# Performance work log

Measured on AMD Instinct MI355X. Metric: run time of the kernel, lower is better.

The kernel has to match this reference:

```python
import jax, jax.numpy as jnp
import numpy as np

N = 32       # number of variables (per-var LSTMs)
L = 128      # window length
D = 128      # hidden dim
HEADS = 8
TAU_MAX = 5
ALPHA = 0.7  # attn_decay_alpha
B = 128      # number of time-ordered windows


def setup_inputs() -> dict:
    key = jax.random.key(0)
    ks = jax.random.split(key, 20)
    s = 0.1
    f = lambda k, shape: (jax.random.normal(k, shape, jnp.float32) * s)
    return {
        "X": jax.random.normal(ks[0], (B, L, N), jnp.float32),
        # per-variable encoder LSTM (input size 1): W_ih (N,4D), W_hh (N,4D,D), combined-style biases kept separate
        "enc_Wih": f(ks[1], (N, 4 * D)),
        "enc_Whh": f(ks[2], (N, 4 * D, D)),
        "enc_b": f(ks[3], (N, 4 * D)),            # b_ih + b_hh merged (mathematically identical)
        "pool_w": f(ks[4], (N, D)),
        "pool_b": f(ks[5], (N,)),
        # shared MultiheadAttention params (torch layout: in_proj (3D,D))
        "in_proj_w": f(ks[6], (3 * D, D)),
        "in_proj_b": f(ks[7], (3 * D,)),
        "out_proj_w": f(ks[8], (D, D)),
        "out_proj_b": f(ks[9], (D,)),
        # per-variable decoder: init_h/init_c Linear(d,d), LSTM(1,d) (input is all-zeros so W_ih drops out), out Linear(d,1)
        "dec_initH_w": f(ks[10], (N, D, D)),
        "dec_initH_b": f(ks[11], (N, D)),
        "dec_initC_w": f(ks[12], (N, D, D)),
        "dec_initC_b": f(ks[13], (N, D)),
        "dec_Whh": f(ks[14], (N, 4 * D, D)),
        "dec_bih": f(ks[15], (N, 4 * D)),
        "dec_bhh": f(ks[16], (N, 4 * D)),
        "dec_out_w": f(ks[17], (N, D)),
        "dec_out_b": f(ks[18], (N,)),
    }


def _lstm_cell(gates, c):
    # torch gate order: i, f, g, o
    i, fg, g, o = jnp.split(gates, 4, axis=-1)
    i = jax.nn.sigmoid(i); fg = jax.nn.sigmoid(fg)
    g = jnp.tanh(g); o = jax.nn.sigmoid(o)
    c = fg * c + i * g
    h = o * jnp.tanh(c)
    return h, c


def _encode(X, Wih, Whh, b, pool_w, pool_b):
    # X: (B,L,N); encoder consumes first L-1 steps of each variable, batched over all N vars
    x = jnp.transpose(X[:, :-1, :], (1, 2, 0))  # (T, N, B)
    Bn = X.shape[0]
    h0 = jnp.zeros((N, Bn, D), X.dtype)

    def step(carry, x_t):  # x_t: (N,B)
        h, c = carry
        gates = (x_t[..., None] * Wih[:, None, :]
                 + jnp.einsum('nbd,ngd->nbg', h, Whh)
                 + b[:, None, :])
        h, c = _lstm_cell(gates, c)
        return (h, c), h

    _, H = jax.lax.scan(step, (h0, h0), x)  # H: (T,N,B,D)
    # TemporalAttnPool: softmax over time of a linear score, weighted sum
    scores = jnp.einsum('tnbd,nd->tnb', H, pool_w) + pool_b[None, :, None]
    a = jax.nn.softmax(scores, axis=0)
    C = jnp.einsum('tnb,tnbd->bnd', a, H)  # (B,N,D)
    return C


def _mha(Q, KV, in_w, in_b, out_w, out_b):
    dh = D // HEADS
    q = Q @ in_w[:D].T + in_b[:D]
    k = KV @ in_w[D:2 * D].T + in_b[D:2 * D]
    v = KV @ in_w[2 * D:].T + in_b[2 * D:]
    sp = lambda x: x.reshape(x.shape[0], x.shape[1], HEADS, dh)
    q, k, v = sp(q), sp(k), sp(v)
    scores = jnp.einsum('bqhd,bkhd->bhqk', q, k) / float(np.sqrt(dh))
    attn = jax.nn.softmax(scores, axis=-1)
    o = jnp.einsum('bhqk,bkhd->bqhd', attn, v).reshape(Q.shape)
    return o @ out_w.T + out_b


def _cross_attend(C, in_w, in_b, out_w, out_b):
    Bn = C.shape[0]
    tmax = min(TAU_MAX, Bn - 1)
    if tmax <= 0:
        return C
    out_sum = jnp.zeros_like(C)
    w_sum = jnp.zeros((Bn, 1, 1), C.dtype)
    for tau in range(1, tmax + 1):  # small fixed loop over lags
        o = _mha(C[tau:], C[:-tau], in_w, in_b, out_w, out_b)
        w = float(np.exp(-ALPHA * (tau - 1)))  # attn_agg == 'decay'
        out_sum = out_sum.at[tau:].add(o * w)
        w_sum = w_sum.at[tau:].add(w)
    out = out_sum / jnp.clip(w_sum, 1e-8)
    return C + out  # residual=True


def _decode(C_star, iHw, iHb, iCw, iCb, Whh, bih, bhh, ow, ob):
    # h0/c0 from tanh(Linear(c_star)); LSTM input is all-zeros so input term reduces to b_ih
    h0 = jnp.tanh(jnp.einsum('bnd,ned->nbe', C_star, iHw) + iHb[:, None, :])
    c0 = jnp.tanh(jnp.einsum('bnd,ned->nbe', C_star, iCw) + iCb[:, None, :])
    b = (bih + bhh)[:, None, :]  # (N,1,4D)

    def step(carry, _):
        h, c = carry
        gates = jnp.einsum('nbd,ngd->nbg', h, Whh) + b
        h, c = _lstm_cell(gates, c)
        o = jnp.einsum('nbd,nd->nb', h, ow) + ob[:, None]
        return (h, c), o

    _, O = jax.lax.scan(step, (h0, c0), None, length=L)  # (L,N,B)
    recon = jnp.transpose(O[:L - 1], (2, 0, 1))  # (B,L-1,N)
    pred = O[L - 1].T                            # (B,N)
    return recon, pred


def reference(X, enc_Wih, enc_Whh, enc_b, pool_w, pool_b,
              in_proj_w, in_proj_b, out_proj_w, out_proj_b,
              dec_initH_w, dec_initH_b, dec_initC_w, dec_initC_b,
              dec_Whh, dec_bih, dec_bhh, dec_out_w, dec_out_b):
    C = _encode(X, enc_Wih, enc_Whh, enc_b, pool_w, pool_b)
    C_star = _cross_attend(C, in_proj_w, in_proj_b, out_proj_w, out_proj_b)
    recon, pred = _decode(C_star, dec_initH_w, dec_initH_b, dec_initC_w, dec_initC_b,
                          dec_Whh, dec_bih, dec_bhh, dec_out_w, dec_out_b)
    return recon, pred, C_star
```

## Files before the change

### kernel.cpp

```cpp
#include <hip/hip_runtime.h>
#include <hip/hip_bf16.h>

typedef unsigned short ushort_t;
typedef unsigned int uint_t;

#define DD   128
#define G4   512
#define BT   16
#define NB   128
#define NV   32

#define OFF_WIH   0
#define OFF_EB    16384
#define OFF_PW    32768
#define OFF_PB    36864
#define OFF_INW   37120
#define OFF_INB   86272
#define OFF_OUTW  86784
#define OFF_OUTB  103168
#define OFF_IHB   103424
#define OFF_ICB   107520
#define OFF_DBIH  111616
#define OFF_DBHH  128000
#define OFF_DOW   144384
#define OFF_DOB   148480
#define P_TOTAL   148736
#define OFF_FLAGS (OFF_PB + 32)

typedef __attribute__((ext_vector_type(8))) short bf16x8;
typedef __attribute__((ext_vector_type(4))) float f32x4;

__device__ __forceinline__ float bf2f(ushort_t u) {
    union { uint_t i; float f; } x; x.i = ((uint_t)u) << 16; return x.f;
}
__device__ __forceinline__ ushort_t f2bf(float f) {
    __hip_bfloat16 h = __float2bfloat16(f);
    return *(ushort_t*)&h;
}
__device__ __forceinline__ float f2u_f(float f) { return f; }
__device__ __forceinline__ uint_t f2u(float f) {
    union { float f; uint_t i; } x; x.f = f; return x.i;
}
__device__ __forceinline__ float u2f(uint_t u) {
    union { uint_t i; float f; } x; x.i = u; return x.f;
}
__device__ __forceinline__ float exp2_f(float x) {
    float r; asm("v_exp_f32 %0, %1" : "=v"(r) : "v"(x)); return r;
}
__device__ __forceinline__ float sigmoid_f(float x) {
    return __builtin_amdgcn_rcpf(1.f + exp2_f(x * -1.442695041f));
}
__device__ __forceinline__ float tanh_f(float x) {
    return 1.f - 2.f * __builtin_amdgcn_rcpf(exp2_f(x * 2.885390082f) + 1.f);
}
__device__ __forceinline__ uint_t cvt_pk_bf16(float a, float b) {
    uint_t r; asm("v_cvt_pk_bf16_f32 %0, %1, %2" : "=v"(r) : "v"(a), "v"(b)); return r;
}
__device__ __forceinline__ bf16x8 pack8(f32x4 a, f32x4 b) {
    union { uint_t u[4]; bf16x8 v; } x;
    x.u[0] = cvt_pk_bf16(a.x, a.y); x.u[1] = cvt_pk_bf16(a.z, a.w);
    x.u[2] = cvt_pk_bf16(b.x, b.y); x.u[3] = cvt_pk_bf16(b.z, b.w);
    return x.v;
}
__device__ __forceinline__ float swz_bcast_l15(float v) {
    return u2f((uint_t)__builtin_amdgcn_ds_swizzle((int)f2u(v), 0x000F));
}
__device__ __forceinline__ void store_out(void* out, long idx, float v, int bf) {
    if (bf) ((ushort_t*)out)[idx] = f2bf(v);
    else    ((float*)out)[idx]    = v;
}
#define LBAR() do { asm volatile("s_waitcnt lgkmcnt(0)" ::: "memory"); \
                    __builtin_amdgcn_s_barrier(); } while (0)

__device__ __forceinline__ int wave_probe(const void* p, int elems) {
    int cap = elems < 2048 ? elems : 2048;
    int lane = threadIdx.x & 63;
    const ushort_t* u = (const ushort_t*)p;
    int cnt = 0, tot = 0;
    for (int j = lane; j < cap; j += 64) {
        ushort_t x = u[j];
        float af = fabsf(bf2f(x));
        tot++;
        if (x == 0 || (af > 1e-7f && af < 100.f)) cnt++;
    }
    #pragma unroll
    for (int off = 32; off >= 1; off >>= 1) {
        cnt += __shfl_xor(cnt, off);
        tot += __shfl_xor(tot, off);
    }
    return (cnt * 10 >= tot * 9) ? 1 : 0;
}

struct Ptr19 { const void* p[19]; };

__global__ __launch_bounds__(256) void prep_kernel(Ptr19 a, float* __restrict__ P,
                                                   float* __restrict__ Xc) {
    __shared__ float tile[32][65];
    if (blockIdx.x < 581) {
        int base = blockIdx.x * 256;
        int src, o0, size;
        if      (base < OFF_EB)   { src = 1;  o0 = base - OFF_WIH;  size = 16384; }
        else if (base < OFF_PW)   { src = 3;  o0 = base - OFF_EB;   size = 16384; }
        else if (base < OFF_PB)   { src = 4;  o0 = base - OFF_PW;   size = 4096;  }
        else if (base < OFF_INW)  { src = 5;  o0 = base - OFF_PB;   size = 32;    }
        else if (base < OFF_INB)  { src = 6;  o0 = base - OFF_INW;  size = 49152; }
        else if (base < OFF_OUTW) { src = 7;  o0 = base - OFF_INB;  size = 384;   }
        else if (base < OFF_OUTB) { src = 8;  o0 = base - OFF_OUTW; size = 16384; }
        else if (base < OFF_IHB)  { src = 9;  o0 = base - OFF_OUTB; size = 128;   }
        else if (base < OFF_ICB)  { src = 11; o0 = base - OFF_IHB;  size = 4096;  }
        else if (base < OFF_DBIH) { src = 13; o0 = base - OFF_ICB;  size = 4096;  }
        else if (base < OFF_DBHH) { src = 15; o0 = base - OFF_DBIH; size = 16384; }
        else if (base < OFF_DOW)  { src = 16; o0 = base - OFF_DBHH; size = 16384; }
        else if (base < OFF_DOB)  { src = 17; o0 = base - OFF_DOW;  size = 4096;  }
        else                      { src = 18; o0 = base - OFF_DOB;  size = 32;    }
        int bf = wave_probe(a.p[src], size);
        int off = o0 + (int)threadIdx.x;
        if (off < size)
            P[base + threadIdx.x] = bf ? bf2f(((const ushort_t*)a.p[src])[off])
                                       : ((const float*)a.p[src])[off];
    } else if (blockIdx.x < 837) {
        int bf = wave_probe(a.p[0], 2048);
        int idx2 = blockIdx.x - 581;
        int bt = (idx2 & 3) * 32, tn0 = (idx2 >> 2) * 64;
        const void* src = a.p[0];
        int tx = threadIdx.x & 63, ty = threadIdx.x >> 6;
        #pragma unroll
        for (int k = 0; k < 8; k++) {
            int row = ty * 8 + k;
            int idx = (bt + row) * 4096 + tn0 + tx;
            tile[row][tx] = bf ? bf2f(((const ushort_t*)src)[idx]) : ((const float*)src)[idx];
        }
        __syncthreads();
        int bx = threadIdx.x & 31, tyy = threadIdx.x >> 5;
        #pragma unroll
        for (int k = 0; k < 8; k++) {
            int tn = tn0 + tyy * 8 + k;
            int t = tn >> 5, nn = tn & 31;
            Xc[t * 4096 + nn * 128 + bt + bx] = tile[bx][tyy * 8 + k];
        }
    } else {
        int which = blockIdx.x - 837;
        int src = (which == 0) ? 0 : (which == 1) ? 2 : (which == 2) ? 10
                : (which == 3) ? 12 : 14;
        int flag = wave_probe(a.p[src], 2048);
        if (threadIdx.x == 0) P[OFF_FLAGS + which] = (float)flag;
    }
}

__global__ __launch_bounds__(512, 2) void enc_kernel(
    const float* __restrict__ Xc, const void* __restrict__ Wraw,
    const float* __restrict__ P, float* __restrict__ Cout)
{
    const int n = blockIdx.y, b0 = blockIdx.x * BT;
    const int tid = threadIdx.x;
    const int w = tid >> 6, lane = tid & 63;
    const int l15 = lane & 15, quad = lane >> 4;
    const int wbf = P[OFF_FLAGS + 1] > 0.5f;
    const int bown = b0 + l15;

    __shared__ alignas(16) ushort_t hS[2][16 * 136];
    for (int i = tid; i < 16 * 136; i += 512) hS[0][i] = 0;

    bf16x8 afrag[4][4];
    #pragma unroll
    for (int typ = 0; typ < 4; typ++) {
        const int g = typ * 128 + 16 * w + l15;
        #pragma unroll
        for (int kc = 0; kc < 4; kc++) {
            const int base = (n * G4 + g) * DD + 32 * kc + 8 * quad;
            if (wbf) {
                afrag[typ][kc] = *(const bf16x8*)((const ushort_t*)Wraw + base);
            } else {
                const float* fp = (const float*)Wraw + base;
                afrag[typ][kc] = pack8(*(const f32x4*)fp, *(const f32x4*)(fp + 4));
            }
        }
    }

    bf16x8 pfrag[4];
    #pragma unroll
    for (int kc = 0; kc < 4; kc++) {
        bf16x8 tmp;
        #pragma unroll
        for (int j = 0; j < 8; j++)
            tmp[j] = (l15 == 0 || l15 == 8)
                   ? (short)f2bf(P[OFF_PW + n * DD + 32 * kc + 8 * quad + j]) : (short)0;
        pfrag[kc] = tmp;
    }

    f32x4 bias4[4], wih4[4];
    #pragma unroll
    for (int typ = 0; typ < 4; typ++) {
        int base = n * G4 + typ * 128 + 16 * w + 4 * quad;
        bias4[typ] = *(const f32x4*)&P[OFF_EB + base];
        wih4[typ]  = *(const f32x4*)&P[OFF_WIH + base];
    }
    const float pb_r = P[OFF_PB + n];
    const f32x4 pb4 = {pb_r, pb_r, pb_r, pb_r};

    float cst[4] = {0.f, 0.f, 0.f, 0.f};
    f32x4 hprev = {0.f, 0.f, 0.f, 0.f};
    f32x4 Cacc  = {0.f, 0.f, 0.f, 0.f};
    float lR = 0.f;

    const float* xnext = Xc + n * 128 + bown;
    float xq = *xnext;
    xnext += 4096;

#define ENC_STEP(T, RB)                                                              \
    do {                                                                             \
        LBAR();                                                                      \
        bf16x8 bh[4];                                                                \
        _Pragma("unroll")                                                            \
        for (int kc = 0; kc < 4; kc++)                                               \
            bh[kc] = *(const bf16x8*)&hS[RB][l15 * 136 + 32 * kc + 8 * quad];        \
        f32x4 xv = {xq, xq, xq, xq};                                                 \
        f32x4 acc[4];                                                                \
        _Pragma("unroll")                                                            \
        for (int typ = 0; typ < 4; typ++)                                            \
            acc[typ] = __builtin_amdgcn_mfma_f32_16x16x32_bf16(                      \
                afrag[typ][0], bh[0], bias4[typ] + xv * wih4[typ], 0, 0, 0);         \
        f32x4 accP = __builtin_amdgcn_mfma_f32_16x16x32_bf16(pfrag[0], bh[0], pb4, 0, 0, 0); \
        xq = *xnext; xnext += 4096;    \
        _Pragma("unroll")                                                            \
        for (int kc = 1; kc < 4; kc++) {                                             \
            accP = __builtin_amdgcn_mfma_f32_16x16x32_bf16(pfrag[kc], bh[kc], accP, 0, 0, 0); \
            _Pragma("unroll")                                                        \
            for (int typ = 0; typ < 4; typ++)                                        \
                acc[typ] = __builtin_amdgcn_mfma_f32_16x16x32_bf16(afrag[typ][kc], bh[kc], acc[typ], 0, 0, 0); \
        }                                                                            \
        if ((T) > 0) {                                                               \
            float e = __expf(swz_bcast_l15(accP[0]));                                \
            lR += e;                                                                 \
            f32x4 ev = {e, e, e, e};                                                 \
            Cacc += ev * hprev;                                                      \
        }                                                                            \
        float hh[4];                                                                 \
        _Pragma("unroll")                                                            \
        for (int r = 0; r < 4; r++) {                                                \
            float ii = sigmoid_f(acc[0][r]);                                         \
            float ff = sigmoid_f(acc[1][r]);                                         \
            float g2 = tanh_f(acc[2][r]);                                            \
            float oo = sigmoid_f(acc[3][r]);                                         \
            float cc = ff * cst[r] + ii * g2;                                        \
            cst[r] = cc;                                                             \
            hh[r] = oo * tanh_f(cc);                                                 \
        }                                                                            \
        hprev.x = hh[0]; hprev.y = hh[1]; hprev.z = hh[2]; hprev.w = hh[3];          \
        uint2 hw;                                                                    \
        hw.x = cvt_pk_bf16(hh[0], hh[1]);                                            \
        hw.y = cvt_pk_bf16(hh[2], hh[3]);                                            \
        *(uint2*)&hS[(RB) ^ 1][l15 * 136 + 16 * w + 4 * quad] = hw;                  \
    } while (0)

    for (int tp = 0; tp < 63; tp++) {
        ENC_STEP(2 * tp, 0);
        ENC_STEP(2 * tp + 1, 1);
    }
    ENC_STEP(126, 0);
#undef ENC_STEP

    LBAR();
    {
        f32x4 accP = __builtin_amdgcn_mfma_f32_16x16x32_bf16(
            pfrag[0], *(const bf16x8*)&hS[1][l15 * 136 + 8 * quad], pb4, 0, 0, 0);
        #pragma unroll
        for (int kc = 1; kc < 4; kc++) {
            bf16x8 bh = *(const bf16x8*)&hS[1][l15 * 136 + 32 * kc + 8 * quad];
            accP = __builtin_amdgcn_mfma_f32_16x16x32_bf16(pfrag[kc], bh, accP, 0, 0, 0);
        }
        float e = __expf(swz_bcast_l15(accP[0]));
        lR += e;
        f32x4 ev = {e, e, e, e};
        Cacc += ev * hprev;
    }
    float inv = 1.f / lR;
    f32x4 iv = {inv, inv, inv, inv};
    f32x4 cv = Cacc * iv;
    *(f32x4*)&Cout[bown * (NV * DD) + n * DD + 16 * w + 4 * quad] = cv;
}

__global__ __launch_bounds__(256) void qkv_kernel(
    const float* __restrict__ C, const float* __restrict__ P,
    float* __restrict__ q, float* __restrict__ k, float* __restrict__ v)
{
    int b = blockIdx.x, p = blockIdx.y, tid = threadIdx.x;
    int j = tid & 127, half = tid >> 7;
    __shared__ float Cb[NV * DD];
    for (int i = tid; i < NV * DD; i += 256) Cb[i] = C[b * (NV * DD) + i];
    __syncthreads();

    const float* wrow = P + OFF_INW + (p * DD + j) * DD;
    float bias = P[OFF_INB + p * DD + j];
    float acc[16];
    #pragma unroll
    for (int nn = 0; nn < 16; nn++) acc[nn] = bias;

    for (int dc = 0; dc < DD; dc += 8) {
        float4 w0 = *(const float4*)&wrow[dc];
        float4 w1 = *(const float4*)&wrow[dc + 4];
        #pragma unroll
        for (int nn = 0; nn < 16; nn++) {
            const float* cb = &Cb[(half * 16 + nn) * DD + dc];
            float4 c0 = *(float4*)&cb[0];
            float4 c1 = *(float4*)&cb[4];
            acc[nn] += c0.x * w0.x + c0.y * w0.y + c0.z * w0.z + c0.w * w0.w
                     + c1.x * w1.x + c1.y * w1.y + c1.z * w1.z + c1.w * w1.w;
        }
    }
    float* dst = (p == 0) ? q : (p == 1) ? k : v;
    for (int nn = 0; nn < 16; nn++)
        dst[b * (NV * DD) + (half * 16 + nn) * DD + j] = acc[nn];
}

__global__ __launch_bounds__(128) void attn_kernel(
    const float* __restrict__ q, const float* __restrict__ k, const float* __restrict__ v,
    const float* __restrict__ C, const float* __restrict__ P,
    float* __restrict__ Cstar, void* __restrict__ dout)
{
    int b = blockIdx.x, half = blockIdx.y, tid = threadIdx.x;
    int obf = P[OFF_FLAGS + 0] > 0.5f;
    int n0 = half * 16;
    __shared__ float Qs[16 * DD], Ks[NV * DD], Vs[NV * DD];
    float* Os = Ks;
    for (int i = tid; i < 16 * DD; i += 128) Qs[i] = q[b * (NV * DD) + n0 * DD + i];
    __syncthreads();

    int hh = tid >> 4, qi = tid & 15;
    float qreg[16];
    #pragma unroll
    for (int u = 0; u < 4; u++) {
        float4 t4 = *(float4*)&Qs[qi * DD + hh * 16 + 4 * u];
        qreg[4*u] = t4.x; qreg[4*u+1] = t4.y; qreg[4*u+2] = t4.z; qreg[4*u+3] = t4.w;
    }

    float Oacc[16];
    #pragma unroll
    for (int u = 0; u < 16; u++) Oacc[u] = 0.f;
    float wsum = 0.f;
    int tmax = (b < 5) ? b : 5;

    for (int tau = 1; tau <= tmax; tau++) {
        __syncthreads();
        for (int i = tid; i < NV * DD; i += 128) {
            Ks[i] = k[(b - tau) * (NV * DD) + i];
            Vs[i] = v[(b - tau) * (NV * DD) + i];
        }
        __syncthreads();

        float s[NV];
        #pragma unroll
        for (int kk = 0; kk < NV; kk++) {
            float a = 0.f;
            #pragma unroll
            for (int u = 0; u < 4; u++) {
                float4 kv = *(float4*)&Ks[kk * DD + hh * 16 + 4 * u];
                a += qreg[4*u] * kv.x + qreg[4*u+1] * kv.y
                   + qreg[4*u+2] * kv.z + qreg[4*u+3] * kv.w;
            }
            s[kk] = a * 0.25f;
        }
        float mm = s[0];
        #pragma unroll
        for (int kk = 1; kk < NV; kk++) mm = fmaxf(mm, s[kk]);
        float ssum = 0.f;
        #pragma unroll
        for (int kk = 0; kk < NV; kk++) { s[kk] = __expf(s[kk] - mm); ssum += s[kk]; }
        float wdk = __expf(-0.7f * (float)(tau - 1));
        wsum += wdk;
        float wr = wdk / ssum;
        #pragma unroll
        for (int u = 0; u < 4; u++) {
            float ax = 0.f, ay = 0.f, az = 0.f, aw = 0.f;
            #pragma unroll
            for (int kk = 0; kk < NV; kk++) {
                float4 vv = *(float4*)&Vs[kk * DD + hh * 16 + 4 * u];
                ax += s[kk] * vv.x; ay += s[kk] * vv.y;
                az += s[kk] * vv.z; aw += s[kk] * vv.w;
            }
            Oacc[4*u] += wr * ax; Oacc[4*u+1] += wr * ay;
            Oacc[4*u+2] += wr * az; Oacc[4*u+3] += wr * aw;
        }
    }

    __syncthreads();
    float winv = (b > 0) ? 1.f / wsum : 0.f;
    #pragma unroll
    for (int u = 0; u < 16; u++)
        Os[qi * DD + hh * 16 + u] = Oacc[u] * winv;
    __syncthreads();

    int j = tid;
    const float* wrow = P + OFF_OUTW + j * DD;
    float obias = P[OFF_OUTB + j];
    for (int nn = 0; nn < 16; nn++) {
        float a = (b > 0) ? obias : 0.f;
        for (int dc = 0; dc < DD; dc += 8) {
            float4 w0 = *(const float4*)&wrow[dc];
            float4 w1 = *(const float4*)&wrow[dc + 4];
            float4 o0 = *(float4*)&Os[nn * DD + dc];
            float4 o1 = *(float4*)&Os[nn * DD + dc + 4];
            a += o0.x*w0.x + o0.y*w0.y + o0.z*w0.z + o0.w*w0.w
               + o1.x*w1.x + o1.y*w1.y + o1.z*w1.z + o1.w*w1.w;
        }
        int nng = n0 + nn;
        float cs = C[b * (NV * DD) + nng * DD + j] + a;
        Cstar[b * (NV * DD) + nng * DD + j] = cs;
        store_out(dout, 524288 + b * (NV * DD) + nng * DD + j, cs, obf);
    }
}

__global__ __launch_bounds__(512, 2) void dec_kernel(
    const float* __restrict__ Cstar,
    const void* __restrict__ iHw, const void* __restrict__ iCw,
    const void* __restrict__ Wraw,
    const float* __restrict__ P, void* __restrict__ out)
{
    const int n = blockIdx.y, b0 = blockIdx.x * BT;
    const int tid = threadIdx.x;
    const int w = tid >> 6, lane = tid & 63;
    const int l15 = lane & 15, quad = lane >> 4;
    const int obf = P[OFF_FLAGS + 0] > 0.5f;
    const int hbf = P[OFF_FLAGS + 2] > 0.5f;
    const int cbf = P[OFF_FLAGS + 3] > 0.5f;
    const int wbf = P[OFF_FLAGS + 4] > 0.5f;
    const int bown = b0 + l15;

    __shared__ alignas(16) ushort_t hS[2][16 * 136];

    bf16x8 cstB[4];
    #pragma unroll
    for (int kc = 0; kc < 4; kc++) {
        const float* cp = &Cstar[bown * (NV * DD) + n * DD + 32 * kc + 8 * quad];
        cstB[kc] = pack8(*(const f32x4*)&cp[0], *(const f32x4*)&cp[4]);
    }
    float cst[4];
    {
        f32x4 hAcc = *(const f32x4*)&P[OFF_IHB + n * DD + 16 * w + 4 * quad];
        f32x4 cAcc = *(const f32x4*)&P[OFF_ICB + n * DD + 16 * w + 4 * quad];
        #pragma unroll
        for (int kc = 0; kc < 4; kc++) {
            const int base = (n * DD + 16 * w + l15) * DD + 32 * kc + 8 * quad;
            bf16x8 wA;
            if (hbf) wA = *(const bf16x8*)((const ushort_t*)iHw + base);
            else {
                const float* fp = (const float*)iHw + base;
                wA = pack8(*(const f32x4*)fp, *(const f32x4*)(fp + 4));
            }
            hAcc = __builtin_amdgcn_mfma_f32_16x16x32_bf16(wA, cstB[kc], hAcc, 0, 0, 0);
            if (cbf) wA = *(const bf16x8*)((const ushort_t*)iCw + base);
            else {
                const float* fp = (const float*)iCw + base;
                wA = pack8(*(const f32x4*)fp, *(const f32x4*)(fp + 4));
            }
            cAcc = __builtin_amdgcn_mfma_f32_16x16x32_bf16(wA, cstB[kc], cAcc, 0, 0, 0);
        }
        float h0 = tanh_f(hAcc[0]), h1 = tanh_f(hAcc[1]);
        float h2 = tanh_f(hAcc[2]), h3 = tanh_f(hAcc[3]);
        #pragma unroll
        for (int r = 0; r < 4; r++) cst[r] = tanh_f(cAcc[r]);
        uint2 hw;
        hw.x = cvt_pk_bf16(h0, h1);
        hw.y = cvt_pk_bf16(h2, h3);
        *(uint2*)&hS[0][l15 * 136 + 16 * w + 4 * quad] = hw;
    }

    bf16x8 afrag[4][4];
    #pragma unroll
    for (int typ = 0; typ < 4; typ++) {
        const int g = typ * 128 + 16 * w + l15;
        #pragma unroll
        for (int kc = 0; kc < 4; kc++) {
            const int base = (n * G4 + g) * DD + 32 * kc + 8 * quad;
            if (wbf) {
                afrag[typ][kc] = *(const bf16x8*)((const ushort_t*)Wraw + base);
            } else {
                const float* fp = (const float*)Wraw + base;
                afrag[typ][kc] = pack8(*(const f32x4*)fp, *(const f32x4*)(fp + 4));
            }
        }
    }

    bf16x8 pfrag[4];
    #pragma unroll
    for (int kc = 0; kc < 4; kc++) {
        bf16x8 tmp;
        #pragma unroll
        for (int j = 0; j < 8; j++)
            tmp[j] = (l15 == 0) ? (short)f2bf(P[OFF_DOW + n * DD + 32 * kc + 8 * quad + j]) : (short)0;
        pfrag[kc] = tmp;
    }

    f32x4 bias4[4];
    #pragma unroll
    for (int typ = 0; typ < 4; typ++) {
        int base = n * G4 + typ * 128 + 16 * w + 4 * quad;
        f32x4 b1 = *(const f32x4*)&P[OFF_DBIH + base];
        f32x4 b2 = *(const f32x4*)&P[OFF_DBHH + base];
        bias4[typ] = b1 + b2;
    }
    const float ob_r = P[OFF_DOB + n];
    const f32x4 ob4 = {ob_r, ob_r, ob_r, ob_r};

#define DEC_STEP(T, RB)                                                              \
    do {                                                                             \
        LBAR();                                                                      \
        bf16x8 bh[4];                                                                \
        _Pragma("unroll")                                                            \
        for (int kc = 0; kc < 4; kc++)                                               \
            bh[kc] = *(const bf16x8*)&hS[RB][l15 * 136 + 32 * kc + 8 * quad];        \
        f32x4 acc[4];                                                                \
        _Pragma("unroll")                                                            \
        for (int typ = 0; typ < 4; typ++)                                            \
            acc[typ] = __builtin_amdgcn_mfma_f32_16x16x32_bf16(afrag[typ][0], bh[0], bias4[typ], 0, 0, 0); \
        _Pragma("unroll")                                                            \
        for (int kc = 1; kc < 4; kc++)                                               \
            _Pragma("unroll")                                                        \
            for (int typ = 0; typ < 4; typ++)                                        \
                acc[typ] = __builtin_amdgcn_mfma_f32_16x16x32_bf16(afrag[typ][kc], bh[kc], acc[typ], 0, 0, 0); \
        if (w == ((T) & 7)) {    \
            f32x4 accP = __builtin_amdgcn_mfma_f32_16x16x32_bf16(pfrag[0], bh[0], ob4, 0, 0, 0); \
            _Pragma("unroll")                                                        \
            for (int kc = 1; kc < 4; kc++)                                           \
                accP = __builtin_amdgcn_mfma_f32_16x16x32_bf16(pfrag[kc], bh[kc], accP, 0, 0, 0); \
            if ((T) > 0 && quad == 0)                                                \
                store_out(out, (long)bown * 4064 + (long)((T) - 1) * NV + n, accP[0], obf); \
        }                                                                            \
        float hh[4];                                                                 \
        _Pragma("unroll")                                                            \
        for (int r = 0; r < 4; r++) {                                                \
            float ii = sigmoid_f(acc[0][r]);                                         \
            float ff = sigmoid_f(acc[1][r]);                                         \
            float g2 = tanh_f(acc[2][r]);                                            \
            float oo = sigmoid_f(acc[3][r]);                                         \
            float cc = ff * cst[r] + ii * g2;                                        \
            cst[r] = cc;                                                             \
            hh[r] = oo * tanh_f(cc);                                                 \
        }                                                                            \
        uint2 hw;                                                                    \
        hw.x = cvt_pk_bf16(hh[0], hh[1]);                                            \
        hw.y = cvt_pk_bf16(hh[2], hh[3]);                                            \
        *(uint2*)&hS[(RB) ^ 1][l15 * 136 + 16 * w + 4 * quad] = hw;                  \
    } while (0)

    for (int tp = 0; tp < 64; tp++) {
        DEC_STEP(2 * tp, 0);
        DEC_STEP(2 * tp + 1, 1);
    }
#undef DEC_STEP

    LBAR();
    if (w == 0) {
        f32x4 accP = __builtin_amdgcn_mfma_f32_16x16x32_bf16(
            pfrag[0], *(const bf16x8*)&hS[0][l15 * 136 + 8 * quad], ob4, 0, 0, 0);
        #pragma unroll
        for (int kc = 1; kc < 4; kc++) {
            bf16x8 bh = *(const bf16x8*)&hS[0][l15 * 136 + 32 * kc + 8 * quad];
            accP = __builtin_amdgcn_mfma_f32_16x16x32_bf16(pfrag[kc], bh, accP, 0, 0, 0);
        }
        if (quad == 0)
            store_out(out, 520192 + (long)bown * NV + n, accP[0], obf);
    }
}

extern "C" void kernel_launch(void* const* d_in, const int* in_sizes, int n_in,
                              void* d_out, int out_size, void* d_ws, size_t ws_size,
                              hipStream_t stream) {
    char* ws = (char*)d_ws;
    float*    P    = (float*)(ws + 0);
    float*    Xc   = (float*)(ws + (1u << 20));
    float*    C    = (float*)(ws + (3u << 20));
    float*    qb   = (float*)(ws + (5u << 20));
    float*    kb   = (float*)(ws + (7u << 20));
    float*    vb   = (float*)(ws + (9u << 20));
    float*    Cst  = (float*)(ws + (11u << 20));

    Ptr19 a;
    for (int i = 0; i < 19; i++) a.p[i] = d_in[i];

    prep_kernel<<<842, 256, 0, stream>>>(a, P, Xc);
    enc_kernel<<<dim3(8, 32), 512, 0, stream>>>(Xc, d_in[2], P, C);
    qkv_kernel<<<dim3(128, 3), 256, 0, stream>>>(C, P, qb, kb, vb);
    attn_kernel<<<dim3(128, 2), 128, 0, stream>>>(qb, kb, vb, C, P, Cst, d_out);
    dec_kernel<<<dim3(8, 32), 512, 0, stream>>>(Cst, d_in[10], d_in[12], d_in[14], P, d_out);
}
```

Before: 420.7 us.

## Compute pooling/output projections from fp32 hidden state via LDS atomics

Replaces the per-step MFMA-based pooling score (encoder) and output projection (decoder) with a per-lane fp32 dot product over each wave's own hidden slice, reduced by lane shuffles and LDS atomicAdd into a triple-buffered scratch row. The result is consumed one step later after the existing barrier. This removes the extra MFMA chain and the register fragments it needed from the serial recurrence. In exchange it adds shared-memory atomics and a rotating zero/accumulate/read buffer scheme. The projection now uses fp32 instead of bf16-rounded h, which changes rounding slightly.

Result: slower. 460.1 us (+9.4%).

```diff
diff --git a/kernel.cpp b/kernel.cpp
--- a/kernel.cpp
+++ b/kernel.cpp
@@ -37,7 +37,6 @@
     __hip_bfloat16 h = __float2bfloat16(f);
     return *(ushort_t*)&h;
 }
-__device__ __forceinline__ float f2u_f(float f) { return f; }
 __device__ __forceinline__ uint_t f2u(float f) {
     union { float f; uint_t i; } x; x.f = f; return x.i;
 }
@@ -61,9 +60,6 @@
     x.u[0] = cvt_pk_bf16(a.x, a.y); x.u[1] = cvt_pk_bf16(a.z, a.w);
     x.u[2] = cvt_pk_bf16(b.x, b.y); x.u[3] = cvt_pk_bf16(b.z, b.w);
     return x.v;
-}
-__device__ __forceinline__ float swz_bcast_l15(float v) {
-    return u2f((uint_t)__builtin_amdgcn_ds_swizzle((int)f2u(v), 0x000F));
 }
 __device__ __forceinline__ void store_out(void* out, long idx, float v, int bf) {
     if (bf) ((ushort_t*)out)[idx] = f2bf(v);
@@ -159,7 +155,9 @@
     const int bown = b0 + l15;
 
     __shared__ alignas(16) ushort_t hS[2][16 * 136];
+    __shared__ float sb[3][16];
     for (int i = tid; i < 16 * 136; i += 512) hS[0][i] = 0;
+    if (tid < 48) ((float*)sb)[tid] = 0.f;
 
     bf16x8 afrag[4][4];
     #pragma unroll
@@ -177,17 +175,6 @@
         }
     }
 
-    bf16x8 pfrag[4];
-    #pragma unroll
-    for (int kc = 0; kc < 4; kc++) {
-        bf16x8 tmp;
-        #pragma unroll
-        for (int j = 0; j < 8; j++)
-            tmp[j] = (l15 == 0 || l15 == 8)
-                   ? (short)f2bf(P[OFF_PW + n * DD + 32 * kc + 8 * quad + j]) : (short)0;
-        pfrag[kc] = tmp;
-    }
-
     f32x4 bias4[4], wih4[4];
     #pragma unroll
     for (int typ = 0; typ < 4; typ++) {
@@ -196,13 +183,15 @@
         wih4[typ]  = *(const f32x4*)&P[OFF_WIH + base];
     }
     const float pb_r = P[OFF_PB + n];
-    const f32x4 pb4 = {pb_r, pb_r, pb_r, pb_r};
+    const f32x4 pw4 = *(const f32x4*)&P[OFF_PW + n * DD + 16 * w + 4 * quad];
 
     float cst[4] = {0.f, 0.f, 0.f, 0.f};
     f32x4 hprev = {0.f, 0.f, 0.f, 0.f};
     f32x4 Cacc  = {0.f, 0.f, 0.f, 0.f};
     float lR = 0.f;
 
+    int sR = 2, sA = 0, sZ = 1;
+
     const float* xnext = Xc + n * 128 + bown;
     float xq = *xnext;
     xnext += 4096;
@@ -210,31 +199,31 @@
 #define ENC_STEP(T, RB)                                                              \
     do {                                                                             \
         LBAR();                                                                      \
+        float sc_rd = 0.f;                                                           \
+        if ((T) > 0) sc_rd = sb[sR][l15];     \
         bf16x8 bh[4];                                                                \
         _Pragma("unroll")                                                            \
         for (int kc = 0; kc < 4; kc++)                                               \
             bh[kc] = *(const bf16x8*)&hS[RB][l15 * 136 + 32 * kc + 8 * quad];        \
-        f32x4 xv = {xq, xq, xq, xq};                                                 \
-        f32x4 acc[4];                                                                \
-        _Pragma("unroll")                                                            \
-        for (int typ = 0; typ < 4; typ++)                                            \
-            acc[typ] = __builtin_amdgcn_mfma_f32_16x16x32_bf16(                      \
-                afrag[typ][0], bh[0], bias4[typ] + xv * wih4[typ], 0, 0, 0);         \
-        f32x4 accP = __builtin_amdgcn_mfma_f32_16x16x32_bf16(pfrag[0], bh[0], pb4, 0, 0, 0); \
-        xq = *xnext; xnext += 4096;    \
-        _Pragma("unroll")                                                            \
-        for (int kc = 1; kc < 4; kc++) {                                             \
-            accP = __builtin_amdgcn_mfma_f32_16x16x32_bf16(pfrag[kc], bh[kc], accP, 0, 0, 0); \
-            _Pragma("unroll")                                                        \
-            for (int typ = 0; typ < 4; typ++)                                        \
-                acc[typ] = __builtin_amdgcn_mfma_f32_16x16x32_bf16(afrag[typ][kc], bh[kc], acc[typ], 0, 0, 0); \
-        }                                                                            \
+        if (tid < 16) sb[sZ][tid] = 0.f;                                             \
         if ((T) > 0) {                                                               \
-            float e = __expf(swz_bcast_l15(accP[0]));                                \
+            float e = __expf(pb_r + sc_rd);                                          \
             lR += e;                                                                 \
             f32x4 ev = {e, e, e, e};                                                 \
             Cacc += ev * hprev;                                                      \
         }                                                                            \
+        f32x4 xv = {xq, xq, xq, xq};                                                 \
+        f32x4 acc[4];                                                                \
+        _Pragma("unroll")                                                            \
+        for (int typ = 0; typ < 4; typ++)                                            \
+            acc[typ] = __builtin_amdgcn_mfma_f32_16x16x32_bf16(                      \
+                afrag[typ][0], bh[0], bias4[typ] + xv * wih4[typ], 0, 0, 0);         \
+        xq = *xnext; xnext += 4096;    \
+        _Pragma("unroll")                                                            \
+        for (int kc = 1; kc < 4; kc++)                                               \
+            _Pragma("unroll")                                                        \
+            for (int typ = 0; typ < 4; typ++)                                        \
+                acc[typ] = __builtin_amdgcn_mfma_f32_16x16x32_bf16(afrag[typ][kc], bh[kc], acc[typ], 0, 0, 0); \
         float hh[4];                                                                 \
         _Pragma("unroll")                                                            \
         for (int r = 0; r < 4; r++) {                                                \
@@ -247,10 +236,16 @@
             hh[r] = oo * tanh_f(cc);                                                 \
         }                                                                            \
         hprev.x = hh[0]; hprev.y = hh[1]; hprev.z = hh[2]; hprev.w = hh[3];          \
+         \
+        float sp = pw4.x * hh[0] + pw4.y * hh[1] + pw4.z * hh[2] + pw4.w * hh[3];    \
+        sp += __shfl_xor(sp, 16);                                                    \
+        sp += __shfl_xor(sp, 32);                                                    \
+        if (quad == 0) atomicAdd(&sb[sA][l15], sp);                                  \
         uint2 hw;                                                                    \
         hw.x = cvt_pk_bf16(hh[0], hh[1]);                                            \
         hw.y = cvt_pk_bf16(hh[2], hh[3]);                                            \
         *(uint2*)&hS[(RB) ^ 1][l15 * 136 + 16 * w + 4 * quad] = hw;                  \
+        int rot = sR; sR = sA; sA = sZ; sZ = rot;                                    \
     } while (0)
 
     for (int tp = 0; tp < 63; tp++) {
@@ -262,14 +257,7 @@
 
     LBAR();
     {
-        f32x4 accP = __builtin_amdgcn_mfma_f32_16x16x32_bf16(
-            pfrag[0], *(const bf16x8*)&hS[1][l15 * 136 + 8 * quad], pb4, 0, 0, 0);
-        #pragma unroll
-        for (int kc = 1; kc < 4; kc++) {
-            bf16x8 bh = *(const bf16x8*)&hS[1][l15 * 136 + 32 * kc + 8 * quad];
-            accP = __builtin_amdgcn_mfma_f32_16x16x32_bf16(pfrag[kc], bh, accP, 0, 0, 0);
-        }
-        float e = __expf(swz_bcast_l15(accP[0]));
+        float e = __expf(pb_r + sb[sR][l15]);
         lR += e;
         f32x4 ev = {e, e, e, e};
         Cacc += ev * hprev;
@@ -427,6 +415,8 @@
     const int bown = b0 + l15;
 
     __shared__ alignas(16) ushort_t hS[2][16 * 136];
+    __shared__ float osb[3][16];
+    if (tid < 48) ((float*)osb)[tid] = 0.f;
 
     bf16x8 cstB[4];
     #pragma unroll
@@ -481,16 +471,6 @@
         }
     }
 
-    bf16x8 pfrag[4];
-    #pragma unroll
-    for (int kc = 0; kc < 4; kc++) {
-        bf16x8 tmp;
-        #pragma unroll
-        for (int j = 0; j < 8; j++)
-            tmp[j] = (l15 == 0) ? (short)f2bf(P[OFF_DOW + n * DD + 32 * kc + 8 * quad + j]) : (short)0;
-        pfrag[kc] = tmp;
-    }
-
     f32x4 bias4[4];
     #pragma unroll
     for (int typ = 0; typ < 4; typ++) {
@@ -500,15 +480,22 @@
         bias4[typ] = b1 + b2;
     }
     const float ob_r = P[OFF_DOB + n];
-    const f32x4 ob4 = {ob_r, ob_r, ob_r, ob_r};
+    const f32x4 ow4 = *(const f32x4*)&P[OFF_DOW + n * DD + 16 * w + 4 * quad];
+
+    int sR = 2, sA = 0, sZ = 1;
 
 #define DEC_STEP(T, RB)                                                              \
     do {                                                                             \
         LBAR();                                                                      \
+        if ((T) > 0 && w == 0 && quad == 0) {    \
+            float ov = osb[sR][l15] + ob_r;                                          \
+            store_out(out, (long)bown * 4064 + (long)((T) - 1) * NV + n, ov, obf);   \
+        }                                                                            \
         bf16x8 bh[4];                                                                \
         _Pragma("unroll")                                                            \
         for (int kc = 0; kc < 4; kc++)                                               \
             bh[kc] = *(const bf16x8*)&hS[RB][l15 * 136 + 32 * kc + 8 * quad];        \
+        if (tid < 16) osb[sZ][tid] = 0.f;                                            \
         f32x4 acc[4];                                                                \
         _Pragma("unroll")                                                            \
         for (int typ = 0; typ < 4; typ++)                                            \
@@ -518,14 +505,6 @@
             _Pragma("unroll")                                                        \
             for (int typ = 0; typ < 4; typ++)                                        \
                 acc[typ] = __builtin_amdgcn_mfma_f32_16x16x32_bf16(afrag[typ][kc], bh[kc], acc[typ], 0, 0, 0); \
-        if (w == ((T) & 7)) {    \
-            f32x4 accP = __builtin_amdgcn_mfma_f32_16x16x32_bf16(pfrag[0], bh[0], ob4, 0, 0, 0); \
-            _Pragma("unroll")                                                        \
-            for (int kc = 1; kc < 4; kc++)                                           \
-                accP = __builtin_amdgcn_mfma_f32_16x16x32_bf16(pfrag[kc], bh[kc], accP, 0, 0, 0); \
-            if ((T) > 0 && quad == 0)                                                \
-                store_out(out, (long)bown * 4064 + (long)((T) - 1) * NV + n, accP[0], obf); \
-        }                                                                            \
         float hh[4];                                                                 \
         _Pragma("unroll")                                                            \
         for (int r = 0; r < 4; r++) {                                                \
@@ -537,10 +516,16 @@
             cst[r] = cc;                                                             \
             hh[r] = oo * tanh_f(cc);                                                 \
         }                                                                            \
+           \
+        float sp = ow4.x * hh[0] + ow4.y * hh[1] + ow4.z * hh[2] + ow4.w * hh[3];    \
+        sp += __shfl_xor(sp, 16);                                                    \
+        sp += __shfl_xor(sp, 32);                                                    \
+        if (quad == 0) atomicAdd(&osb[sA][l15], sp);                                 \
         uint2 hw;                                                                    \
         hw.x = cvt_pk_bf16(hh[0], hh[1]);                                            \
         hw.y = cvt_pk_bf16(hh[2], hh[3]);                                            \
         *(uint2*)&hS[(RB) ^ 1][l15 * 136 + 16 * w + 4 * quad] = hw;                  \
+        int rot = sR; sR = sA; sA = sZ; sZ = rot;                                    \
     } while (0)
 
     for (int tp = 0; tp < 64; tp++) {
@@ -550,16 +535,9 @@
 #undef DEC_STEP
 
     LBAR();
-    if (w == 0) {
-        f32x4 accP = __builtin_amdgcn_mfma_f32_16x16x32_bf16(
-            pfrag[0], *(const bf16x8*)&hS[0][l15 * 136 + 8 * quad], ob4, 0, 0, 0);
-        #pragma unroll
-        for (int kc = 1; kc < 4; kc++) {
-            bf16x8 bh = *(const bf16x8*)&hS[0][l15 * 136 + 32 * kc + 8 * quad];
-            accP = __builtin_amdgcn_mfma_f32_16x16x32_bf16(pfrag[kc], bh, accP, 0, 0, 0);
-        }
-        if (quad == 0)
-            store_out(out, 520192 + (long)bown * NV + n, accP[0], obf);
+    if (w == 0 && quad == 0) {
+        float ov = osb[sR][l15] + ob_r;
+        store_out(out, 520192 + (long)bown * NV + n, ov, obf);
     }
 }
 
```
